# Kernel optimization log

Hardware: AMD Instinct MI355X
Metric: run time of the kernel (lower is better)

## Reference

```python
import jax, jax.numpy as jnp
import numpy as np

EMB = 1024
FFN = 4096
H = 16
HD = EMB // H
EPS = 1e-6
SLOPE = 0.01


def leaky_relu(x):
    return jnp.where(x >= 0, x, SLOPE * x)


def layer_norm(x, g, b):
    mu = jnp.mean(x, axis=-1, keepdims=True)
    var = jnp.mean((x - mu) ** 2, axis=-1, keepdims=True)
    return (x - mu) * jax.lax.rsqrt(var + EPS) * g + b


def setup_inputs() -> dict:
    key = jax.random.key(0)
    ks = jax.random.split(key, 16)
    B, N = 2, 2048
    x = jax.random.normal(ks[0], (B, N, EMB), dtype=jnp.float32)

    def lin(k, fan_in, fan_out, kaiming_normal):
        kw, kb = jax.random.split(k)
        gain = float(np.sqrt(2.0 / (1.0 + SLOPE ** 2)))
        if kaiming_normal:
            W = jax.random.normal(kw, (fan_out, fan_in)) * (gain / np.sqrt(fan_in))
        else:
            bound = gain * np.sqrt(3.0 / fan_in)
            W = jax.random.uniform(kw, (fan_out, fan_in), minval=-bound, maxval=bound)
        b = jax.random.normal(kb, (fan_out,)) * 1e-6
        return W.astype(jnp.float32), b.astype(jnp.float32)

    Wq, bq = lin(ks[1], EMB, EMB, True)
    Wk, bk = lin(ks[2], EMB, EMB, True)
    Wv, bv = lin(ks[3], EMB, EMB, True)
    Wo, bo = lin(ks[4], EMB, EMB, True)
    W1, b1 = lin(ks[5], EMB, FFN, False)
    W2, b2 = lin(ks[6], FFN, EMB, False)
    return {
        "x": x,
        "ln1_g": jnp.ones((EMB,)), "ln1_b": jnp.zeros((EMB,)),
        "ln2_g": jnp.ones((EMB,)), "ln2_b": jnp.zeros((EMB,)),
        "Wq": Wq, "bq": bq, "Wk": Wk, "bk": bk, "Wv": Wv, "bv": bv,
        "Wo": Wo, "bo": bo, "W1": W1, "b1": b1, "W2": W2, "b2": b2,
    }


def reference(x, ln1_g, ln1_b, ln2_g, ln2_b, Wq, bq, Wk, bk, Wv, bv, Wo, bo, W1, b1, W2, b2):
    B, N, _ = x.shape
    h = x
    xn = layer_norm(x, ln1_g, ln1_b)
    # QKV projections, split heads: [B, H, N, HD]
    def heads(t):
        return t.reshape(B, N, H, HD).transpose(0, 2, 1, 3)
    q = heads(xn @ Wq.T + bq)
    k = heads(xn @ Wk.T + bk)
    v = heads(xn @ Wv.T + bv)
    scores = jnp.einsum('bhnd,bhmd->bhnm', q, k) / jnp.sqrt(jnp.float32(HD))
    probs = leaky_relu(scores)  # non-softmax attention
    ctx = jnp.einsum('bhnm,bhmd->bhnd', probs, v)
    ctx = ctx.transpose(0, 2, 1, 3).reshape(B, N, EMB)
    attn_out = ctx @ Wo.T + bo
    x = attn_out + h
    h = x
    xn = layer_norm(x, ln2_g, ln2_b)
    ff = leaky_relu(xn @ W1.T + b1) @ W2.T + b2
    return ff + h
```

## Files before the change

### kernel.cpp

```cpp
#include <hip/hip_runtime.h>
#include <hip/hip_bf16.h>


typedef unsigned short u16;
typedef unsigned int u32;
typedef __bf16 bf16x8 __attribute__((ext_vector_type(8)));
typedef __bf16 bf16x4 __attribute__((ext_vector_type(4)));
typedef float f32x4 __attribute__((ext_vector_type(4)));
typedef unsigned short u16x8 __attribute__((ext_vector_type(8)));
typedef unsigned int u32x2 __attribute__((ext_vector_type(2)));
typedef short s16x4 __attribute__((ext_vector_type(4)));

typedef const __attribute__((address_space(1))) void* as1cv;
typedef __attribute__((address_space(3))) void* as3v;

#define MFMA16(a, b, c) __builtin_amdgcn_mfma_f32_16x16x32_bf16((a), (b), (c), 0, 0, 0)
#define GLL16(g, l) __builtin_amdgcn_global_load_lds((as1cv)(g), (as3v)(l), 16, 0, 0)

__device__ __forceinline__ u16 f2bf(float f) {
  unsigned u = __builtin_bit_cast(unsigned, f);
  u += 0x7fffu + ((u >> 16) & 1u);
  return (u16)(u >> 16);
}
__device__ __forceinline__ float bf2f(u16 u) {
  return __builtin_bit_cast(float, ((unsigned)u) << 16);
}
__device__ __forceinline__ float lrelu(float v) { return fmaxf(v, 0.01f * v); }

__device__ __forceinline__ void mfma16x16(f32x4& c, bf16x4 a, bf16x4 b) {
#if __has_builtin(__builtin_amdgcn_mfma_f32_16x16x16bf16_1k)
  c = __builtin_amdgcn_mfma_f32_16x16x16bf16_1k(
      __builtin_bit_cast(s16x4, a), __builtin_bit_cast(s16x4, b), c, 0, 0, 0);
#else
  u32x2 au = __builtin_bit_cast(u32x2, a);
  u32x2 bu = __builtin_bit_cast(u32x2, b);
  asm volatile("s_nop 2\n\tv_mfma_f32_16x16x16_bf16 %0, %1, %2, %0"
               : "+v"(c) : "v"(au), "v"(bu));
#endif
}

__device__ __forceinline__ int xcds(int bid, int nwg) {
  int cpx = nwg >> 3;
  return (bid & 7) * cpx + (bid >> 3);
}

__global__ __launch_bounds__(256) void cvt6(
    const float* __restrict__ p0, const float* __restrict__ p1,
    const float* __restrict__ p2, const float* __restrict__ p3,
    const float* __restrict__ p4, const float* __restrict__ p5,
    u16* __restrict__ o0, u16* __restrict__ o1, u16* __restrict__ o2,
    u16* __restrict__ o3, u16* __restrict__ o4, u16* __restrict__ o5)
{
  int i = blockIdx.x * 256 + threadIdx.x;
  const float* src; u16* dst; int off;
  if (i < 4 * 131072) {
    int s = i >> 17; off = i & 131071;
    src = (s == 0) ? p0 : (s == 1) ? p1 : (s == 2) ? p2 : p3;
    dst = (s == 0) ? o0 : (s == 1) ? o1 : (s == 2) ? o2 : o3;
  } else {
    int j = i - 4 * 131072;
    int s = j >> 19; off = j & 524287;
    src = s ? p5 : p4;
    dst = s ? o5 : o4;
  }
  const float4* s4 = (const float4*)src;
  float4 a = s4[(size_t)off * 2], b = s4[(size_t)off * 2 + 1];
  u16x8 o = { f2bf(a.x), f2bf(a.y), f2bf(a.z), f2bf(a.w),
              f2bf(b.x), f2bf(b.y), f2bf(b.z), f2bf(b.w) };
  *(u16x8*)(dst + (size_t)off * 8) = o;
}

__global__ __launch_bounds__(256) void ln_k(
    const float* __restrict__ x, const float* __restrict__ g,
    const float* __restrict__ bb, u16* __restrict__ out)
{
  const int tid = threadIdx.x;
  const int row = blockIdx.x;
  const float4* xr = (const float4*)(x + (size_t)row * 1024);
  float4 v = xr[tid];
  float s  = v.x + v.y + v.z + v.w;
  float s2 = v.x*v.x + v.y*v.y + v.z*v.z + v.w*v.w;
#pragma unroll
  for (int o = 32; o > 0; o >>= 1) { s += __shfl_down(s, o, 64); s2 += __shfl_down(s2, o, 64); }
  __shared__ float sh[8];
  if ((tid & 63) == 0) { sh[tid >> 6] = s; sh[4 + (tid >> 6)] = s2; }
  __syncthreads();
  s  = sh[0] + sh[1] + sh[2] + sh[3];
  s2 = sh[4] + sh[5] + sh[6] + sh[7];
  float mu  = s * (1.0f / 1024.0f);
  float var = s2 * (1.0f / 1024.0f) - mu * mu;
  float rs  = rsqrtf(var + 1e-6f);
  float4 gv = ((const float4*)g)[tid];
  float4 bv = ((const float4*)bb)[tid];
  ushort4 o;
  o.x = f2bf((v.x - mu) * rs * gv.x + bv.x);
  o.y = f2bf((v.y - mu) * rs * gv.y + bv.y);
  o.z = f2bf((v.z - mu) * rs * gv.z + bv.z);
  o.w = f2bf((v.w - mu) * rs * gv.w + bv.w);
  ((ushort4*)out)[(size_t)row * 256 + tid] = o;
}

__device__ __forceinline__ void gemm_core128(
    const u16* __restrict__ A, const u16* __restrict__ W,
    int kstride, int klen,
    int row0, int wrow0, u16* lsA, u16* lsB, f32x4 (&acc)[4][4])
{
  const int tid  = threadIdx.x;
  const int lane = tid & 63, wave = tid >> 6;
  const int wr = wave >> 1, wc = wave & 1;
  const int lr = lane & 15, lg = lane >> 4;

  const u16* ga0 = A + (size_t)(row0 + (tid >> 2)) * kstride + (tid & 3) * 8;
  const u16* ga1 = ga0 + (size_t)64 * kstride;
  const u16* gb0 = W + (size_t)(wrow0 + (tid >> 2)) * kstride + (tid & 3) * 8;
  const u16* gb1 = gb0 + (size_t)64 * kstride;
  u16* la = lsA + tid * 8;
  u16* lb = lsB + tid * 8;

#define GSTAGE(buf)                                                  \
  {                                                                  \
    GLL16(ga0, la + (buf) * 4096);                                   \
    GLL16(ga1, la + (buf) * 4096 + 2048);                            \
    GLL16(gb0, lb + (buf) * 4096);                                   \
    GLL16(gb1, lb + (buf) * 4096 + 2048);                            \
    ga0 += 32; ga1 += 32; gb0 += 32; gb1 += 32;                      \
  }

  const int nsteps = klen >> 5;
  GSTAGE(0); GSTAGE(1);

  int bi = 0;
  int bs = 2;
  for (int t = 0; t < nsteps; t++) {
    if (t + 1 < nsteps) asm volatile("s_waitcnt vmcnt(4)" ::: "memory");
    else                asm volatile("s_waitcnt vmcnt(0)" ::: "memory");
    __builtin_amdgcn_s_barrier();
    asm volatile("" ::: "memory");
    if (t + 2 < nsteps) { GSTAGE(bs); bs = (bs == 2) ? 0 : bs + 1; }

    const u16* cA = lsA + bi * 4096;
    const u16* cB = lsB + bi * 4096;
    bf16x8 av[4], bv[4];
#pragma unroll
    for (int mi = 0; mi < 4; mi++)
      av[mi] = *reinterpret_cast<const bf16x8*>(cA + (wr * 64 + mi * 16 + lr) * 32 + lg * 8);
#pragma unroll
    for (int ni = 0; ni < 4; ni++)
      bv[ni] = *reinterpret_cast<const bf16x8*>(cB + (wc * 64 + ni * 16 + lr) * 32 + lg * 8);
#pragma unroll
    for (int mi = 0; mi < 4; mi++)
#pragma unroll
      for (int ni = 0; ni < 4; ni++)
        acc[mi][ni] = MFMA16(av[mi], bv[ni], acc[mi][ni]);
    bi = (bi == 2) ? 0 : bi + 1;
  }
#undef GSTAGE
}

__global__ __launch_bounds__(256, 3) void gemm_qkv(
    const u16* __restrict__ xn,
    const u16* __restrict__ Wq, const u16* __restrict__ Wk, const u16* __restrict__ Wv,
    const float* __restrict__ bq, const float* __restrict__ bk, const float* __restrict__ bv,
    u16* __restrict__ qb, u16* __restrict__ kb, u16* __restrict__ vtb)
{
  __shared__ u16 lsA[3 * 4096];
  __shared__ u16 lsB[3 * 4096];
  const int wid = xcds(blockIdx.x, 768);
  const int mt = wid / 24, nt = wid % 24;
  const int row0 = mt * 128, col0 = nt * 128;
  const int sel = col0 >> 10, c0 = col0 & 1023;
  const u16* W = (sel == 0) ? Wq : (sel == 1) ? Wk : Wv;
  const float* bias = (sel == 0) ? bq : (sel == 1) ? bk : bv;

  f32x4 acc[4][4];
  f32x4 z = {0.f, 0.f, 0.f, 0.f};
#pragma unroll
  for (int mi = 0; mi < 4; mi++)
#pragma unroll
    for (int ni = 0; ni < 4; ni++) acc[mi][ni] = z;

  gemm_core128(xn, W, 1024, 1024, row0, c0, lsA, lsB, acc);

  const int lane = threadIdx.x & 63, wave = threadIdx.x >> 6;
  const int wr = wave >> 1, wc = wave & 1;
  const int lr = lane & 15, lg = lane >> 4;
  const float qscale = (sel == 0) ? 0.125f : 1.0f;
#pragma unroll
  for (int ni = 0; ni < 4; ni++) {
    int c = c0 + wc * 64 + ni * 16 + lr;
    float bsv = bias[c];
    int h = c >> 6, hd = c & 63;
#pragma unroll
    for (int mi = 0; mi < 4; mi++) {
      int rbase = row0 + wr * 64 + mi * 16 + lg * 4;
      int b = rbase >> 11;
      int n = rbase & 2047;
      if (sel < 2) {
        u16* dst = (sel == 0) ? qb : kb;
        size_t base = ((size_t)(b * 16 + h) * 2048 + n) * 64 + hd;
#pragma unroll
        for (int r = 0; r < 4; r++)
          dst[base + (size_t)r * 64] = f2bf((acc[mi][ni][r] + bsv) * qscale);
      } else {
        size_t base = ((size_t)((b * 16 + h) * 64 + hd)) * 2048 + n;
        ushort4 o;
        o.x = f2bf(acc[mi][ni][0] + bsv);
        o.y = f2bf(acc[mi][ni][1] + bsv);
        o.z = f2bf(acc[mi][ni][2] + bsv);
        o.w = f2bf(acc[mi][ni][3] + bsv);
        *(ushort4*)(vtb + base) = o;
      }
    }
  }
}

template <int EPI>
__global__ __launch_bounds__(256, 3) void gemm128(
    const u16* __restrict__ A, const u16* __restrict__ W,
    const float* __restrict__ bias, float* __restrict__ outf,
    u16* __restrict__ outh, const float* __restrict__ extra,
    int K, int nTiles, int nwg)
{
  __shared__ u16 lsA[3 * 4096];
  __shared__ u16 lsB[3 * 4096];
  const int wid = xcds(blockIdx.x, nwg);
  const int mt = wid / nTiles, nt = wid % nTiles;
  const int row0 = mt * 128, col0 = nt * 128;

  f32x4 acc[4][4];
  f32x4 z = {0.f, 0.f, 0.f, 0.f};
#pragma unroll
  for (int mi = 0; mi < 4; mi++)
#pragma unroll
    for (int ni = 0; ni < 4; ni++) acc[mi][ni] = z;

  gemm_core128(A, W, K, K, row0, col0, lsA, lsB, acc);

  const int N = nTiles * 128;
  const int lane = threadIdx.x & 63, wave = threadIdx.x >> 6;
  const int wr = wave >> 1, wc = wave & 1;
  const int lr = lane & 15, lg = lane >> 4;
#pragma unroll
  for (int ni = 0; ni < 4; ni++) {
    int col = col0 + wc * 64 + ni * 16 + lr;
    float bsv = bias[col];
#pragma unroll
    for (int mi = 0; mi < 4; mi++) {
      int rbase = row0 + wr * 64 + mi * 16 + lg * 4;
#pragma unroll
      for (int r = 0; r < 4; r++) {
        float v = acc[mi][ni][r] + bsv;
        size_t idx = (size_t)(rbase + r) * N + col;
        if (EPI == 0) {
          outf[idx] = v + extra[idx];
        } else {
          outh[idx] = f2bf(lrelu(v));
        }
      }
    }
  }
}

__global__ __launch_bounds__(256, 3) void gemm_ffn2(
    const u16* __restrict__ A, const u16* __restrict__ W,
    u16* __restrict__ pout)
{
  __shared__ u16 lsA[3 * 4096];
  __shared__ u16 lsB[3 * 4096];
  const int wid = xcds(blockIdx.x, 1024);
  const int chunk = wid >> 8, rem = wid & 255;
  const int mt = rem >> 3, nt = rem & 7;
  const int row0 = mt * 128, col0 = nt * 128;

  f32x4 acc[4][4];
  f32x4 z = {0.f, 0.f, 0.f, 0.f};
#pragma unroll
  for (int mi = 0; mi < 4; mi++)
#pragma unroll
    for (int ni = 0; ni < 4; ni++) acc[mi][ni] = z;

  gemm_core128(A + chunk * 1024, W + chunk * 1024, 4096, 1024,
               row0, col0, lsA, lsB, acc);

  u16* out = pout + (size_t)chunk * (4096 * 1024);
  const int lane = threadIdx.x & 63, wave = threadIdx.x >> 6;
  const int wr = wave >> 1, wc = wave & 1;
  const int lr = lane & 15, lg = lane >> 4;
#pragma unroll
  for (int ni = 0; ni < 4; ni++) {
    int col = col0 + wc * 64 + ni * 16 + lr;
#pragma unroll
    for (int mi = 0; mi < 4; mi++) {
      int rbase = row0 + wr * 64 + mi * 16 + lg * 4;
#pragma unroll
      for (int r = 0; r < 4; r++)
        out[(size_t)(rbase + r) * 1024 + col] = f2bf(acc[mi][ni][r]);
    }
  }
}

__global__ __launch_bounds__(256) void reduce_ffn2(
    const u16* __restrict__ p, const float* __restrict__ b2,
    const float* __restrict__ x2, float* __restrict__ out)
{
  size_t i = ((size_t)blockIdx.x * 256 + threadIdx.x) * 4;
  int col = (int)(i & 1023);
  ushort4 a0 = *(const ushort4*)(p + i);
  ushort4 a1 = *(const ushort4*)(p + (size_t)(4096 * 1024) + i);
  ushort4 a2 = *(const ushort4*)(p + (size_t)(2 * 4096 * 1024) + i);
  ushort4 a3 = *(const ushort4*)(p + (size_t)(3 * 4096 * 1024) + i);
  float4 bv = *(const float4*)(b2 + col);
  float4 xv = *(const float4*)(x2 + i);
  float4 r;
  r.x = bf2f(a0.x) + bf2f(a1.x) + bf2f(a2.x) + bf2f(a3.x) + bv.x + xv.x;
  r.y = bf2f(a0.y) + bf2f(a1.y) + bf2f(a2.y) + bf2f(a3.y) + bv.y + xv.y;
  r.z = bf2f(a0.z) + bf2f(a1.z) + bf2f(a2.z) + bf2f(a3.z) + bv.z + xv.z;
  r.w = bf2f(a0.w) + bf2f(a1.w) + bf2f(a2.w) + bf2f(a3.w) + bv.w + xv.w;
  *(float4*)(out + i) = r;
}

__global__ __launch_bounds__(256, 3) void attn_k(
    const u16* __restrict__ qb, const u16* __restrict__ kb,
    const u16* __restrict__ vtb, u16* __restrict__ ctx)
{
  __shared__ u16 lds[3 * 8192];

  const int tid = threadIdx.x;
  const int lane = tid & 63, wq = tid >> 6;
  const int lr = lane & 15, lg = lane >> 4;
  const int wid = xcds(blockIdx.x, 512);
  const int bh = wid >> 4, qt = wid & 15;
  const int n0 = qt * 128;
  const u16* qh = qb + (size_t)bh * 2048 * 64;
  const u16* kh = kb + (size_t)bh * 2048 * 64;
  const u16* vh = vtb + (size_t)bh * 64 * 2048;

  const int srow = tid >> 3;
  const int sgg  = (tid & 7) ^ (srow & 7);
  const size_t koff0 = (size_t)srow * 64 + sgg * 8;
  const size_t koff1 = koff0 + (size_t)32 * 64;
  const size_t voff0 = (size_t)srow * 2048 + sgg * 8;
  const size_t voff1 = voff0 + (size_t)32 * 2048;
  const int dk0 = tid * 8, dk1 = tid * 8 + 2048;

#define STAGE_KV(t, jb)                                              \
  {                                                                  \
    const u16* ks_ = kh + (size_t)(t) * 4096;                        \
    const u16* vs_ = vh + (t) * 64;                                  \
    u16* lb_ = lds + (jb) * 8192;                                    \
    GLL16(ks_ + koff0, lb_ + dk0);                                   \
    GLL16(ks_ + koff1, lb_ + dk1);                                   \
    GLL16(vs_ + voff0, lb_ + 4096 + dk0);                            \
    GLL16(vs_ + voff1, lb_ + 4096 + dk1);                            \
  }

  STAGE_KV(0, 0);
  STAGE_KV(1, 1);

  bf16x8 qr[2][2];
#pragma unroll
  for (int qi = 0; qi < 2; qi++)
#pragma unroll
    for (int ks = 0; ks < 2; ks++)
      qr[qi][ks] = *(const bf16x8*)(
          qh + (size_t)(n0 + wq * 32 + qi * 16 + lr) * 64 + ks * 32 + lg * 8);
  asm volatile("" ::: "memory");

  f32x4 z = {0.f, 0.f, 0.f, 0.f};
  f32x4 cacc[4][2];
#pragma unroll
  for (int di = 0; di < 4; di++) { cacc[di][0] = z; cacc[di][1] = z; }

  const int lswz = lr & 7;
  int bi = 0, bs = 2;
  for (int t = 0; t < 32; t++) {
    if (t < 31) asm volatile("s_waitcnt vmcnt(4)" ::: "memory");
    else        asm volatile("s_waitcnt vmcnt(0)" ::: "memory");
    __builtin_amdgcn_s_barrier();
    asm volatile("" ::: "memory");
    if (t + 2 < 32) { STAGE_KV(t + 2, bs); bs = (bs == 2) ? 0 : bs + 1; }

    const u16* lk = lds + bi * 8192;
    const u16* lv = lds + bi * 8192 + 4096;
#pragma unroll
    for (int ki = 0; ki < 4; ki++) {
      f32x4 s0 = z, s1 = z;
#pragma unroll
      for (int ks = 0; ks < 2; ks++) {
        bf16x8 kf = *(const bf16x8*)(
            lk + (ki * 16 + lr) * 64 + (((ks * 4 + lg) ^ lswz) * 8));
        s0 = MFMA16(kf, qr[0][ks], s0);
        s1 = MFMA16(kf, qr[1][ks], s1);
      }
      bf16x4 p0, p1;
#pragma unroll
      for (int r = 0; r < 4; r++) {
        p0[r] = (__bf16)lrelu(s0[r]);
        p1[r] = (__bf16)lrelu(s1[r]);
      }
#pragma unroll
      for (int di = 0; di < 4; di++) {
        bf16x4 vf = *(const bf16x4*)(
            lv + (di * 16 + lr) * 64 +
            (((ki * 2 + (lg >> 1)) ^ lswz) * 8) + (lg & 1) * 4);
        mfma16x16(cacc[di][0], vf, p0);
        mfma16x16(cacc[di][1], vf, p1);
      }
    }
    bi = (bi == 2) ? 0 : bi + 1;
  }

  const int b = bh >> 4, h = bh & 15;
#pragma unroll
  for (int qi = 0; qi < 2; qi++) {
    int n = n0 + wq * 32 + qi * 16 + lr;
    u16* op = ctx + ((size_t)(b * 2048 + n)) * 1024 + h * 64;
#pragma unroll
    for (int di = 0; di < 4; di++) {
      ushort4 o;
      o.x = f2bf(cacc[di][qi][0]);
      o.y = f2bf(cacc[di][qi][1]);
      o.z = f2bf(cacc[di][qi][2]);
      o.w = f2bf(cacc[di][qi][3]);
      *(ushort4*)(op + di * 16 + lg * 4) = o;
    }
  }
#undef STAGE_KV
}

extern "C" void kernel_launch(void* const* d_in, const int* in_sizes, int n_in,
                              void* d_out, int out_size, void* d_ws, size_t ws_size,
                              hipStream_t stream) {
  (void)in_sizes; (void)n_in; (void)out_size; (void)ws_size;
  const float* x    = (const float*)d_in[0];
  const float* ln1g = (const float*)d_in[1];
  const float* ln1b = (const float*)d_in[2];
  const float* ln2g = (const float*)d_in[3];
  const float* ln2b = (const float*)d_in[4];
  const float* Wq = (const float*)d_in[5];  const float* bq = (const float*)d_in[6];
  const float* Wk = (const float*)d_in[7];  const float* bk = (const float*)d_in[8];
  const float* Wv = (const float*)d_in[9];  const float* bv = (const float*)d_in[10];
  const float* Wo = (const float*)d_in[11]; const float* bo = (const float*)d_in[12];
  const float* W1 = (const float*)d_in[13]; const float* b1 = (const float*)d_in[14];
  const float* W2 = (const float*)d_in[15]; const float* b2 = (const float*)d_in[16];

  char* ws = (char*)d_ws;
  u16*   WqB  = (u16*)(ws + ((size_t)0 << 20));
  u16*   WkB  = (u16*)(ws + ((size_t)2 << 20));
  u16*   WvB  = (u16*)(ws + ((size_t)4 << 20));
  u16*   WoB  = (u16*)(ws + ((size_t)6 << 20));
  u16*   W1B  = (u16*)(ws + ((size_t)8 << 20));
  u16*   W2B  = (u16*)(ws + ((size_t)16 << 20));
  u16*   xn1  = (u16*)(ws + ((size_t)24 << 20));
  u16*   qb   = (u16*)(ws + ((size_t)32 << 20));
  u16*   kb   = (u16*)(ws + ((size_t)40 << 20));
  u16*   vtb  = (u16*)(ws + ((size_t)48 << 20));
  u16*   ctxb = (u16*)(ws + ((size_t)56 << 20));
  float* x2   = (float*)(ws + ((size_t)64 << 20));
  u16*   xn2  = (u16*)(ws + ((size_t)80 << 20));
  u16*   ff1  = (u16*)(ws + ((size_t)88 << 20));
  u16*   pF2  = (u16*)(ws + ((size_t)24 << 20));

  dim3 blk(256);

  cvt6<<<dim3(6144), blk, 0, stream>>>(Wq, Wk, Wv, Wo, W1, W2,
                                       WqB, WkB, WvB, WoB, W1B, W2B);
  ln_k<<<dim3(4096), blk, 0, stream>>>(x, ln1g, ln1b, xn1);
  gemm_qkv<<<dim3(768), blk, 0, stream>>>(xn1, WqB, WkB, WvB, bq, bk, bv,
                                          qb, kb, vtb);
  attn_k<<<dim3(512), blk, 0, stream>>>(qb, kb, vtb, ctxb);
  gemm128<0><<<dim3(256), blk, 0, stream>>>(ctxb, WoB, bo, x2, (u16*)nullptr, x,
                                            1024, 8, 256);
  ln_k<<<dim3(4096), blk, 0, stream>>>(x2, ln2g, ln2b, xn2);
  gemm128<1><<<dim3(1024), blk, 0, stream>>>(xn2, W1B, b1, (float*)nullptr, ff1,
                                             (const float*)nullptr, 1024, 32, 1024);
  gemm_ffn2<<<dim3(1024), blk, 0, stream>>>(ff1, W2B, pF2);
  reduce_ffn2<<<dim3(4096), blk, 0, stream>>>(pF2, b2, x2, (float*)d_out);
}
```

Before: 353.8 us.

## Use BK=64 double-buffered GEMM tiles with XOR-swizzled LDS layout

Restructures the shared GEMM core to load 64-wide K slices per stage into two buffers instead of three 32-wide buffers. LDS rows are written and read through an XOR swizzle of the 16-byte groups to avoid bank conflicts. A second barrier per iteration guards buffer reuse before the next prefetch. Launch bounds drop from three to two blocks per CU to fit the larger LDS footprint, which lowers occupancy while halving the number of barrier and wait steps per K.

```diff
diff --git a/kernel.cpp b/kernel.cpp
--- a/kernel.cpp
+++ b/kernel.cpp
@@ -110,61 +110,78 @@
   const int wr = wave >> 1, wc = wave & 1;
   const int lr = lane & 15, lg = lane >> 4;
 
-  const u16* ga0 = A + (size_t)(row0 + (tid >> 2)) * kstride + (tid & 3) * 8;
-  const u16* ga1 = ga0 + (size_t)64 * kstride;
-  const u16* gb0 = W + (size_t)(wrow0 + (tid >> 2)) * kstride + (tid & 3) * 8;
-  const u16* gb1 = gb0 + (size_t)64 * kstride;
+  const int srow = tid >> 3;
+  const int sg   = (tid & 7) ^ (srow & 7);
+  const u16* ga0 = A + (size_t)(row0 +  0 + srow) * kstride + sg * 8;
+  const u16* ga1 = A + (size_t)(row0 + 32 + srow) * kstride + sg * 8;
+  const u16* ga2 = A + (size_t)(row0 + 64 + srow) * kstride + sg * 8;
+  const u16* ga3 = A + (size_t)(row0 + 96 + srow) * kstride + sg * 8;
+  const u16* gb0 = W + (size_t)(wrow0 +  0 + srow) * kstride + sg * 8;
+  const u16* gb1 = W + (size_t)(wrow0 + 32 + srow) * kstride + sg * 8;
+  const u16* gb2 = W + (size_t)(wrow0 + 64 + srow) * kstride + sg * 8;
+  const u16* gb3 = W + (size_t)(wrow0 + 96 + srow) * kstride + sg * 8;
   u16* la = lsA + tid * 8;
   u16* lb = lsB + tid * 8;
 
-#define GSTAGE(buf)                                                  \
-  {                                                                  \
-    GLL16(ga0, la + (buf) * 4096);                                   \
-    GLL16(ga1, la + (buf) * 4096 + 2048);                            \
-    GLL16(gb0, lb + (buf) * 4096);                                   \
-    GLL16(gb1, lb + (buf) * 4096 + 2048);                            \
-    ga0 += 32; ga1 += 32; gb0 += 32; gb1 += 32;                      \
-  }
-
-  const int nsteps = klen >> 5;
+#define GSTAGE(buf)                                                   \
+  {                                                                   \
+    GLL16(ga0, la + (buf) * 8192 + 0 * 2048);                         \
+    GLL16(ga1, la + (buf) * 8192 + 1 * 2048);                         \
+    GLL16(ga2, la + (buf) * 8192 + 2 * 2048);                         \
+    GLL16(ga3, la + (buf) * 8192 + 3 * 2048);                         \
+    GLL16(gb0, lb + (buf) * 8192 + 0 * 2048);                         \
+    GLL16(gb1, lb + (buf) * 8192 + 1 * 2048);                         \
+    GLL16(gb2, lb + (buf) * 8192 + 2 * 2048);                         \
+    GLL16(gb3, lb + (buf) * 8192 + 3 * 2048);                         \
+    ga0 += 64; ga1 += 64; ga2 += 64; ga3 += 64;                       \
+    gb0 += 64; gb1 += 64; gb2 += 64; gb3 += 64;                       \
+  }
+
+  const int nsteps = klen >> 6;
   GSTAGE(0); GSTAGE(1);
 
-  int bi = 0;
-  int bs = 2;
+  const int swzr = lr & 7;
   for (int t = 0; t < nsteps; t++) {
-    if (t + 1 < nsteps) asm volatile("s_waitcnt vmcnt(4)" ::: "memory");
+    if (t + 1 < nsteps) asm volatile("s_waitcnt vmcnt(8)" ::: "memory");
     else                asm volatile("s_waitcnt vmcnt(0)" ::: "memory");
     __builtin_amdgcn_s_barrier();
     asm volatile("" ::: "memory");
-    if (t + 2 < nsteps) { GSTAGE(bs); bs = (bs == 2) ? 0 : bs + 1; }
-
-    const u16* cA = lsA + bi * 4096;
-    const u16* cB = lsB + bi * 4096;
-    bf16x8 av[4], bv[4];
-#pragma unroll
-    for (int mi = 0; mi < 4; mi++)
-      av[mi] = *reinterpret_cast<const bf16x8*>(cA + (wr * 64 + mi * 16 + lr) * 32 + lg * 8);
-#pragma unroll
-    for (int ni = 0; ni < 4; ni++)
-      bv[ni] = *reinterpret_cast<const bf16x8*>(cB + (wc * 64 + ni * 16 + lr) * 32 + lg * 8);
-#pragma unroll
-    for (int mi = 0; mi < 4; mi++)
+
+    const u16* cA = lsA + (t & 1) * 8192;
+    const u16* cB = lsB + (t & 1) * 8192;
+#pragma unroll
+    for (int ks = 0; ks < 2; ks++) {
+      bf16x8 av[4], bv[4];
+#pragma unroll
+      for (int mi = 0; mi < 4; mi++)
+        av[mi] = *reinterpret_cast<const bf16x8*>(
+            cA + (wr * 64 + mi * 16 + lr) * 64 + (((ks * 4 + lg) ^ swzr) * 8));
 #pragma unroll
       for (int ni = 0; ni < 4; ni++)
-        acc[mi][ni] = MFMA16(av[mi], bv[ni], acc[mi][ni]);
-    bi = (bi == 2) ? 0 : bi + 1;
+        bv[ni] = *reinterpret_cast<const bf16x8*>(
+            cB + (wc * 64 + ni * 16 + lr) * 64 + (((ks * 4 + lg) ^ swzr) * 8));
+#pragma unroll
+      for (int mi = 0; mi < 4; mi++)
+#pragma unroll
+        for (int ni = 0; ni < 4; ni++)
+          acc[mi][ni] = MFMA16(av[mi], bv[ni], acc[mi][ni]);
+    }
+
+    __builtin_amdgcn_s_barrier();
+    asm volatile("" ::: "memory");
+    if (t + 2 < nsteps) GSTAGE(t & 1);
   }
 #undef GSTAGE
 }
 
-__global__ __launch_bounds__(256, 3) void gemm_qkv(
+__global__ __launch_bounds__(256, 2) void gemm_qkv(
     const u16* __restrict__ xn,
     const u16* __restrict__ Wq, const u16* __restrict__ Wk, const u16* __restrict__ Wv,
     const float* __restrict__ bq, const float* __restrict__ bk, const float* __restrict__ bv,
     u16* __restrict__ qb, u16* __restrict__ kb, u16* __restrict__ vtb)
 {
-  __shared__ u16 lsA[3 * 4096];
-  __shared__ u16 lsB[3 * 4096];
+  __shared__ u16 lsA[2 * 8192];
+  __shared__ u16 lsB[2 * 8192];
   const int wid = xcds(blockIdx.x, 768);
   const int mt = wid / 24, nt = wid % 24;
   const int row0 = mt * 128, col0 = nt * 128;
@@ -215,14 +232,14 @@
 }
 
 template <int EPI>
-__global__ __launch_bounds__(256, 3) void gemm128(
+__global__ __launch_bounds__(256, 2) void gemm128(
     const u16* __restrict__ A, const u16* __restrict__ W,
     const float* __restrict__ bias, float* __restrict__ outf,
     u16* __restrict__ outh, const float* __restrict__ extra,
     int K, int nTiles, int nwg)
 {
-  __shared__ u16 lsA[3 * 4096];
-  __shared__ u16 lsB[3 * 4096];
+  __shared__ u16 lsA[2 * 8192];
+  __shared__ u16 lsB[2 * 8192];
   const int wid = xcds(blockIdx.x, nwg);
   const int mt = wid / nTiles, nt = wid % nTiles;
   const int row0 = mt * 128, col0 = nt * 128;
@@ -261,12 +278,12 @@
   }
 }
 
-__global__ __launch_bounds__(256, 3) void gemm_ffn2(
+__global__ __launch_bounds__(256, 2) void gemm_ffn2(
     const u16* __restrict__ A, const u16* __restrict__ W,
     u16* __restrict__ pout)
 {
-  __shared__ u16 lsA[3 * 4096];
-  __shared__ u16 lsB[3 * 4096];
+  __shared__ u16 lsA[2 * 8192];
+  __shared__ u16 lsB[2 * 8192];
   const int wid = xcds(blockIdx.x, 1024);
   const int chunk = wid >> 8, rem = wid & 255;
   const int mt = rem >> 3, nt = rem & 7;
```

Result: faster. 333.9 us (-5.6%).
